# Optimization experiments

Hardware: AMD Instinct MI355X
Metric: run time of the kernel (lower is better)

Reference implementation:

```python
import jax, jax.numpy as jnp
import numpy as np

B, T, R, C, H = 8, 176, 116, 64, 200   # batch, time, roi, conv channels, mlp hidden
MAXG = 176                              # pad target for number of groups (== time)
TAU = 1e-4
IU = np.triu_indices(R, 1)              # upper triangle (diagonal=1), row-major like torch mask select


def setup_inputs() -> dict:
    key = jax.random.key(0)
    k = jax.random.split(key, 6)
    # gumbel(0,1) noise, as used by F.gumbel_softmax
    u = jax.random.uniform(k[4], (B, T, T), jnp.float32, 1e-10, 1.0 - 1e-7)
    gumbel = -jnp.log(-jnp.log(u))
    return {
        "X": jax.random.normal(k[0], (B, T, R), jnp.float32),
        "conv_w": jax.random.normal(k[1], (C, R), jnp.float32) * float(1.0 / np.sqrt(R)),
        "conv_b": jnp.zeros((C,), jnp.float32),
        "fc1_w": jax.random.normal(k[2], (H, C), jnp.float32) * float(1.0 / np.sqrt(C)),
        "fc1_b": jnp.zeros((H,), jnp.float32),
        "fc2_w": jax.random.normal(k[3], (1, H), jnp.float32) * float(1.0 / np.sqrt(H)),
        "fc2_b": jnp.zeros((1,), jnp.float32),
        "gumbel": gumbel,
    }


def _per_sample(Xi, idx):
    # Xi: [R, T] (roi x time), idx: [T] soft group index per timepoint
    # toggle(): consecutive runs of equal idx values form groups
    change = jnp.concatenate([jnp.ones((1,), bool), idx[1:] != idx[:-1]])
    gid = jnp.cumsum(change.astype(jnp.int32)) - 1            # [T] group id per timepoint
    num_groups = gid[-1] + 1
    toggle = (gid[None, :] == jnp.arange(MAXG)[:, None]).astype(Xi.dtype)  # [MAXG, T] one-hot rows
    MASK = (idx + 1.0)[None, :] * toggle                       # [MAXG, T]
    inv = jax.lax.stop_gradient(1.0 / MASK.sum(axis=0))        # [T] (detached in torch)
    final = inv[None, :] * MASK                                # [MAXG, T]
    res = Xi[None, :, :] * final[:, None, :]                   # [MAXG, R, T] group-masked signals
    # torch.corrcoef over rows (time axis is observations); normalization constant cancels
    xm = res - res.mean(axis=-1, keepdims=True)
    cov = jnp.einsum('grt,gst->grs', xm, xm)                   # [MAXG, R, R]
    d = jnp.einsum('grt,grt->gr', xm, xm)                      # diag of cov
    denom = jnp.sqrt(d[:, :, None] * d[:, None, :])
    corr = jnp.clip(cov / jnp.where(denom > 0, denom, 1.0), -1.0, 1.0)
    flat = corr[:, IU[0], IU[1]]                               # [MAXG, R*(R-1)/2] upper-tri flatten
    valid = (jnp.arange(MAXG) < num_groups)[:, None]           # zero-pad groups past num_groups
    return jnp.where(valid, flat, 0.0)


def reference(X, conv_w, conv_b, fc1_w, fc1_b, fc2_w, fc2_b, gumbel):
    # Conv1d(kernel_size=1) == per-timepoint linear: [B,T,R] -> [B,T,C]
    out_cnn = jnp.einsum('btr,cr->btc', X, conv_w) + conv_b
    diff = out_cnn[:, :, None, :] - out_cnn[:, None, :, :]      # [B,T,T,C]
    dist = jnp.sqrt(jax.nn.relu(diff * diff) + 1e-9)
    h = jax.nn.relu(jnp.einsum('btsc,hc->btsh', dist, fc1_w) + fc1_b)
    clf = jax.nn.sigmoid(jnp.einsum('btsh,h->bts', h, fc2_w[0]) + fc2_b[0])  # [B,T,T]
    eye = jnp.eye(T, dtype=bool)
    grouping_M = jnp.where(eye[None, :, :], 1.0, clf)
    # eigh returns ascending eigenvalues; torch sorts descending (reverse), but S uses the
    # ORIGINAL (un-reordered) eigenvectors, matching the source exactly
    vals, vecs = jnp.linalg.eigh(grouping_M)
    vals_desc = vals[:, ::-1]
    vals_desc = jnp.where(vals_desc <= 0, 1e-7, vals_desc)
    S = vecs * jnp.sqrt(vals_desc)[:, None, :] * 1000.0         # vectors @ diag(sqrt(vals)) * 1000
    Group = jax.nn.softmax((S + gumbel) / TAU, axis=2)          # gumbel_softmax, tau=1e-4, soft
    soft_indices = jnp.sum(Group * jnp.arange(T, dtype=S.dtype), axis=-1)  # [B,T]
    Xp = jnp.transpose(X, (0, 2, 1))                            # [B,R,T]
    padded = jax.vmap(_per_sample)(Xp, soft_indices)            # [B, MAXG, R*(R-1)/2]
    return padded, grouping_M, soft_indices
```

## Files before the change

kernel.cpp:

```cpp
#include <hip/hip_runtime.h>
#pragma clang fp contract(off)

#define Bn 8
#define Tn 176
#define Rn 116
#define Cn 64
#define Hn 200
#define NPAIRn 6670
#define MAXGn 176
#define TAUf 1e-4f
#define LD 176
#define LDA 177
#define LEAF 22
#define NT 512
#define FEPS 5.9604645e-08f
#define FEPS2 3.5527137e-15f
#define FSAFMIN 1.17549435e-38f

static __device__ __forceinline__ float f_sign(float a, float b) {
  return (b >= 0.0f) ? fabsf(a) : -fabsf(a);
}
static __device__ __forceinline__ float f_lapy2(float x, float y) {
  float xa = fabsf(x), ya = fabsf(y);
  float w = fmaxf(xa, ya), z = fminf(xa, ya);
  if (z == 0.0f) return w;
  float q = z / w;
  return w * sqrtf(1.0f + q * q);
}
static __device__ void f_lartg(float f, float g, float* c, float* s, float* r) {
  if (g == 0.0f) { *c = 1.0f; *s = 0.0f; *r = f; }
  else if (f == 0.0f) { *c = 0.0f; *s = (g >= 0.0f) ? 1.0f : -1.0f; *r = fabsf(g); }
  else {
    float d = sqrtf(f * f + g * g);
    float rr = (f >= 0.0f) ? d : -d;
    *c = f / rr; *s = g / rr; *r = rr;
  }
}
static __device__ float f_snrm2_strided(const float* x, int n, int stride) {
  float scale = 0.0f, ssq = 1.0f;
  for (int i = 0; i < n; i++) {
    float ax = fabsf(x[i * stride]);
    if (ax != 0.0f) {
      if (scale < ax) {
        float q = scale / ax;
        ssq = 1.0f + ssq * (q * q);
// ... 604 lines not shown
          g = d[i] - p;
          r = (d[i + 1] - g) * s + 2.0f * c * bb;
          p = s * r;
          d[i] = g + p;
          g = c * r - bb;
          work_c[i] = c; work_s[i] = s;
        }
        for (int j = 1; j <= l - mm; ++j) {
          float cj = work_c[mm + j - 1], sj = work_s[mm + j - 1];
          for (int rr = 0; rr < n; rr++) {
            float t1 = Z[rr * ldz + mm + j], t0 = Z[rr * ldz + mm + j - 1];
            Z[rr * ldz + mm + j] = cj * t1 - sj * t0;
            Z[rr * ldz + mm + j - 1] = sj * t1 + cj * t0;
          }
        }
        d[l] -= p; e[l - 1] = g;
      }
    }
  }
  for (int ii = 1; ii < n; ++ii) {
    int i = ii - 1, k = i; float p = d[i];
    for (int j = ii; j < n; ++j) if (d[j] < p) { k = j; p = d[j]; }
    if (k != i) {
      d[k] = d[i]; d[i] = p;
      for (int r = 0; r < n; r++) { float t = Z[r * ldz + i]; Z[r * ldz + i] = Z[r * ldz + k]; Z[r * ldz + k] = t; }
    }
  }
}

static __device__ void laed1_f(int tid, int nb, int n1, int off, float rho_in,
    float* Zb, float* Qt, float* Um, float* dd,
    float* dlamda, float* w2, float* lamv, float* wtv, float* zv, float* dnew, float* dsort,
    int* indxq, int* indxp, int* indxc, int* indxm,
    float* shs, int* shi) {
  int n2 = nb - n1;
  if (tid == 0) {
    float rho = rho_in;
    for (int i = 0; i < n1; i++) zv[i] = Zb[(off + n1 - 1) * LD + off + i];
    for (int i = 0; i < n2; i++) zv[n1 + i] = Zb[(off + n1) * LD + off + n1 + i];
    if (rho < 0.0f) for (int i = n1; i < nb; i++) zv[i] = -zv[i];
    const float isq2 = 0.70710678118654752440f;
    for (int i = 0; i < nb; i++) zv[i] *= isq2;
    rho = fabsf(2.0f * rho);
    for (int i = n1; i < nb; i++) indxq[off + i] += n1;
    for (int i = 0; i < nb; i++) dsort[i] = dd[off + indxq[off + i]];
    f_lamrg(n1, n2, dsort, 1, 1, indxc);
    for (int i = 0; i < nb; i++) indxm[i] = indxq[off + indxc[i]];
    float zmax = 0.0f, dmax = 0.0f;
    for (int i = 0; i < nb; i++) {
      float az = fabsf(zv[i]); if (az > zmax) zmax = az;
      float ad = fabsf(dd[off + i]); if (ad > dmax) dmax = ad;
    }
    float tol = 8.0f * FEPS * ((dmax > zmax) ? dmax : zmax);
    int K = 0;
    if (rho * zmax <= tol) {
      for (int j = 0; j < nb; j++) indxp[j] = indxm[j];
    } else {
      int K2 = nb; int pj = 0; int j; bool found = false;
      for (j = 0; j < nb; j++) {
        int nj = indxm[j];
        if (rho * fabsf(zv[nj]) <= tol) { K2--; indxp[K2] = nj; if (j == nb - 1) break; }
        else { pj = nj; found = true; break; }
      }
      if (found) {
        while (true) {
          j++;
          if (j >= nb) break;
          int nj = indxm[j];
          if (rho * fabsf(zv[nj]) <= tol) { K2--; indxp[K2] = nj; }
          else {
            float s_ = zv[pj], c_ = zv[nj];
            float tau_ = f_lapy2(c_, s_);
            float t_ = dd[off + nj] - dd[off + pj];
            c_ /= tau_; s_ = -s_ / tau_;
            if (fabsf(t_ * c_ * s_) <= tol) {
              zv[nj] = tau_; zv[pj] = 0.0f;
              for (int r = 0; r < nb; r++) {
                float x = Zb[(off + r) * LD + off + pj], y = Zb[(off + r) * LD + off + nj];
                Zb[(off + r) * LD + off + pj] = c_ * x + s_ * y;
                Zb[(off + r) * LD + off + nj] = c_ * y - s_ * x;
              }
              float t2 = dd[off + pj] * c_ * c_ + dd[off + nj] * s_ * s_;
              dd[off + nj] = dd[off + pj] * s_ * s_ + dd[off + nj] * c_ * c_;
              dd[off + pj] = t2;
              K2--;
              int i_ = 1;
              while (true) {
                if (K2 + i_ < nb) {
                  if (dd[off + pj] < dd[off + indxp[K2 + i_]]) {
                    indxp[K2 + i_ - 1] = indxp[K2 + i_]; indxp[K2 + i_] = pj; i_++;
                  } else { indxp[K2 + i_ - 1] = pj; break; }
                } else { indxp[K2 + i_ - 1] = pj; break; }
              }
              pj = nj;
            } else {
              dlamda[K] = dd[off + pj]; w2[K] = zv[pj]; indxp[K] = pj; K++;
              pj = nj;
            }
          }
        }
        dlamda[K] = dd[off + pj]; w2[K] = zv[pj]; indxp[K] = pj; K++;
      }
    }
    shi[0] = K; shs[0] = rho;
  }
  __syncthreads();
  int K = shi[0]; float rho = shs[0];
  if (K == 0) {
    for (int idx = tid; idx < nb * nb; idx += NT) {
      int r = idx / nb, jj = idx - r * nb;
      Qt[r * LD + jj] = Zb[(off + r) * LD + off + indxp[jj]];
    }
    for (int jj = tid; jj < nb; jj += NT) dnew[jj] = dd[off + indxp[jj]];
    __syncthreads();
    for (int idx = tid; idx < nb * nb; idx += NT) {
      int r = idx / nb, jj = idx - r * nb;
      Zb[(off + r) * LD + off + jj] = Qt[r * LD + jj];
    }
    for (int jj = tid; jj < nb; jj += NT) { dd[off + jj] = dnew[jj]; indxq[off + jj] = jj; }
    __syncthreads();
    return;
  }
  if (K == 1) {
    if (tid == 0) { lamv[0] = dlamda[0] + rho * w2[0] * w2[0]; Um[0] = 1.0f; }
  } else if (K == 2) {
    if (tid < 2) {
      float u0, u1, dl_;
      f_laed5(tid, dlamda, w2, rho, &dl_, &u0, &u1);
      lamv[tid] = dl_; Um[0 * LD + tid] = u0; Um[1 * LD + tid] = u1;
    }
  } else {
    if (tid < K) laed4_net(K, tid, dlamda, w2, rho, &lamv[tid], &Um[tid]);
  }
  __syncthreads();
  if (K > 2) {
    if (tid < K) {
      int i = tid; float val = Um[i * LD + i];
      for (int j2 = 0; j2 < K; j2++) if (j2 != i) val *= Um[i * LD + j2] / (dlamda[i] - dlamda[j2]);
      wtv[i] = f_sign(sqrtf(fabsf(val)), w2[i]);
    }
    __syncthreads();
    if (tid < K) {
      int j2 = tid;
      for (int i = 0; i < K; i++) Um[i * LD + j2] = wtv[i] / Um[i * LD + j2];
      float nrm = f_snrm2_strided(&Um[j2], K, LD);
      for (int i = 0; i < K; i++) Um[i * LD + j2] /= nrm;
    }
    __syncthreads();
  }
  for (int idx = tid; idx < nb * K; idx += NT) {
    int r = idx / K, j2 = idx - r * K;
    float acc = 0.0f;
    for (int i = 0; i < K; i++) acc = fmaf(Zb[(off + r) * LD + off + indxp[i]], Um[i * LD + j2], acc);
    Qt[r * LD + j2] = acc;
  }
  int nd = nb - K;
  for (int idx = tid; idx < nb * nd; idx += NT) {
    int r = idx / nd, jj = idx - r * nd;
    Qt[r * LD + K + jj] = Zb[(off + r) * LD + off + indxp[K + jj]];
  }
  for (int jj = tid; jj < nb; jj += NT) dnew[jj] = (jj < K) ? lamv[jj] : dd[off + indxp[jj]];
  __syncthreads();
  for (int idx = tid; idx < nb * nb; idx += NT) {
    int r = idx / nb, jj = idx - r * nb;
    Zb[(off + r) * LD + off + jj] = Qt[r * LD + jj];
  }
  for (int jj = tid; jj < nb; jj += NT) dd[off + jj] = dnew[jj];
  __syncthreads();
  if (tid == 0) f_lamrg(K, nb - K, dnew, 1, -1, indxq + off);
  __syncthreads();
}

#define FSTR 109824
__global__ __launch_bounds__(NT) void k_eigh2(const float* __restrict__ gm,
    float* __restrict__ fws,
    float* __restrict__ vecsbt, float* __restrict__ scales) {
  int b = blockIdx.x, tid = threadIdx.x;
  extern __shared__ char dynsm[];
  float* A = (float*)dynsm;
  float* sm1 = A + Tn * LDA;
  int* ib_ = (int*)(sm1 + 1760);
  float* Zb = fws + (size_t)b * FSTR;
  float* Qt = Zb + 30976;
  float* Um = Qt + 30976;
  float* Wp = Um + 30976;
  float* Wa = Wp + 5632;
  float* Wb = Wa + 5632;
  float* dd = sm1;
  float* ee = sm1 + 176;
  float* tauv = sm1 + 352;
  float* dlamda = sm1 + 528;
  float* w2 = sm1 + 704;
  float* lamv = sm1 + 880;
  float* wtv = sm1 + 1056;
  float* zv = sm1 + 1232;
  float* dnew = sm1 + 1408;
  float* dsort = sm1 + 1584;
  int* indxq = ib_;
  int* indxp = ib_ + 176;
  int* indxc = ib_ + 352;
  int* indxm = ib_ + 528;
  __shared__ float shv[176];
  __shared__ float shs[2];
  __shared__ int shi[2];
  __shared__ float t12[64];
  __shared__ float Tm[1024];
  __shared__ float Zleaf[8][LEAF][LEAF + 1];
  for (int i = tid; i < Tn * Tn; i += NT)
    A[(i / Tn) * LDA + (i % Tn)] = gm[(size_t)b * Tn * Tn + i];
  __syncthreads();
  for (int i0 = 0; i0 < Tn - 32; i0 += 32) {
    for (int i = 0; i < 32; i++) {
      int g = i0 + i;
      if (i > 0) {
        for (int r = g + tid; r < Tn; r += NT) {
          float acc = A[r * LDA + g];
          for (int k = 0; k < i; k++) acc = fmaf(-Wp[g * 32 + k], A[r * LDA + (i0 + k)], acc);
          for (int k = 0; k < i; k++) acc = fmaf(-A[g * LDA + (i0 + k)], Wp[r * 32 + k], acc);
          A[r * LDA + g] = acc;
        }
        __syncthreads();
      }
      if (tid == 0) {
        float scale = 0.0f, ssq = 1.0f;
        for (int r = g + 2; r < Tn; r++) {
          float ax = fabsf(A[r * LDA + g]);
          if (ax != 0.0f) {
            if (scale < ax) { float q = scale / ax; ssq = 1.0f + ssq * (q * q); scale = ax; }
            else { float q = ax / scale; ssq = ssq + q * q; }
          }
        }
        float xnorm = scale * sqrtf(ssq);
        float alpha = A[(g + 1) * LDA + g];
        float taui = 0.0f, scal = 0.0f;
        if (xnorm == 0.0f) { ee[g] = alpha; }
        else {
          float beta = -f_sign(f_lapy2(alpha, xnorm), alpha);
          taui = (beta - alpha) / beta;
          scal = 1.0f / (alpha - beta);
          ee[g] = beta;
        }
        tauv[g] = taui; shs[0] = taui; shs[1] = scal;
      }
      __syncthreads();
      float taui = shs[0];
      if (taui != 0.0f) {
        float scal = shs[1];
        for (int r = g + 2 + tid; r < Tn; r += NT) A[r * LDA + g] *= scal;
      }
      __syncthreads();
      if (tid == 0) A[(g + 1) * LDA + g] = 1.0f;
      __syncthreads();
      for (int r = g + 1 + tid; r < Tn; r += NT) {
        float acc = 0.0f;
        for (int c = g + 1; c < r; c++) acc = fmaf(A[c * LDA + g], A[r * LDA + c], acc);
        acc = fmaf(A[r * LDA + g], A[r * LDA + r], acc);
        float temp2 = 0.0f;
        for (int k = r + 1; k < Tn; k++) temp2 = fmaf(A[k * LDA + r], A[k * LDA + g], temp2);
        acc += temp2;
        shv[r] = acc;
      }
      __syncthreads();
      if (i > 0) {
        if (tid < i) {
          int k = tid;
          float acc = 0.0f;
          for (int r = g + 1; r < Tn; r++) acc = fmaf(Wp[r * 32 + k], A[r * LDA + g], acc);
          t12[k] = acc;
        }
        __syncthreads();
        for (int r = g + 1 + tid; r < Tn; r += NT) {
          float acc = shv[r];
          for (int k = 0; k < i; k++) acc = fmaf(-t12[k], A[r * LDA + (i0 + k)], acc);
          shv[r] = acc;
        }
        __syncthreads();
        if (tid < i) {
          int k = tid;
          float acc = 0.0f;
          for (int r = g + 1; r < Tn; r++) acc = fmaf(A[r * LDA + (i0 + k)], A[r * LDA + g], acc);
          t12[32 + k] = acc;
        }
        __syncthreads();
        for (int r = g + 1 + tid; r < Tn; r += NT) {
          float acc = shv[r];
          for (int k = 0; k < i; k++) acc = fmaf(-t12[32 + k], Wp[r * 32 + k], acc);
          shv[r] = acc;
        }
        __syncthreads();
      }
      for (int r = g + 1 + tid; r < Tn; r += NT) shv[r] = taui * shv[r];
      __syncthreads();
      if (tid == 0) {
        float dot = 0.0f;
        for (int r = g + 1; r < Tn; r++) dot = fmaf(shv[r], A[r * LDA + g], dot);
        shs[0] = -0.5f * taui * dot;
      }
      __syncthreads();
      float alf = shs[0];
      for (int r = g + 1 + tid; r < Tn; r += NT) Wp[r * 32 + i] = fmaf(alf, A[r * LDA + g], shv[r]);
      __syncthreads();
    }
    {
      int base2 = i0 + 32;
      int nt2 = Tn - base2;
      int npr = nt2 * (nt2 + 1) / 2;
      for (int p = tid; p < npr; p += NT) {
        int rr = (int)((sqrtf(8.0f * (float)p + 1.0f) - 1.0f) * 0.5f);
        while ((rr + 1) * (rr + 2) / 2 <= p) rr++;
        while (rr * (rr + 1) / 2 > p) rr--;
        int cc = p - rr * (rr + 1) / 2;
        int r = base2 + rr, c = base2 + cc;
        float acc = A[r * LDA + c];
        for (int L = 0; L < 32; L++) {
          acc = fmaf(A[r * LDA + (i0 + L)], -Wp[c * 32 + L], acc);
          acc = fmaf(Wp[r * 32 + L], -A[c * LDA + (i0 + L)], acc);
        }
        A[r * LDA + c] = acc;
        if (r != c) A[c * LDA + r] = acc;
      }
      __syncthreads();
      if (tid < 32) {
        int g2 = i0 + tid;
        A[(g2 + 1) * LDA + g2] = ee[g2];
      }
      __syncthreads();
    }
  }
  for (int i = 160; i < Tn - 1; i++) {
    if (tid == 0) {
      float scale = 0.0f, ssq = 1.0f;
      for (int r = i + 2; r < Tn; r++) {
        float ax = fabsf(A[r * LDA + i]);
        if (ax != 0.0f) {
          if (scale < ax) { float q = scale / ax; ssq = 1.0f + ssq * (q * q); scale = ax; }
          else { float q = ax / scale; ssq = ssq + q * q; }
        }
      }
      float xnorm = scale * sqrtf(ssq);
      float alpha = A[(i + 1) * LDA + i];
      float taui = 0.0f, scal = 0.0f;
      if (xnorm == 0.0f) { ee[i] = alpha; }
      else {
        float beta = -f_sign(f_lapy2(alpha, xnorm), alpha);
        taui = (beta - alpha) / beta;
        scal = 1.0f / (alpha - beta);
        ee[i] = beta;
      }
      tauv[i] = taui; shs[0] = taui; shs[1] = scal;
    }
    __syncthreads();
    float taui = shs[0];
    if (taui != 0.0f) {
      float scal = shs[1];
      for (int r = i + 2 + tid; r < Tn; r += NT) A[r * LDA + i] *= scal;
      __syncthreads();
      for (int r = i + 1 + tid; r < Tn; r += NT) {
        float acc = 0.0f;
        for (int c = i + 1; c < r; c++) {
          float vc = (c == i + 1) ? 1.0f : A[c * LDA + i];
          acc = fmaf(taui * vc, A[r * LDA + c], acc);
        }
        float vr = (r == i + 1) ? 1.0f : A[r * LDA + i];
        acc = fmaf(taui * vr, A[r * LDA + r], acc);
        float temp2 = 0.0f;
        for (int k = r + 1; k < Tn; k++) temp2 = fmaf(A[k * LDA + r], A[k * LDA + i], temp2);
        acc = fmaf(taui, temp2, acc);
        shv[r] = acc;
      }
      __syncthreads();
      if (tid == 0) {
        float dot = 0.0f;
        for (int r = i + 1; r < Tn; r++) {
          float vr = (r == i + 1) ? 1.0f : A[r * LDA + i];
          dot = fmaf(vr, shv[r], dot);
        }
        shs[0] = -0.5f * taui * dot;
      }
      __syncthreads();
      float alpha2 = shs[0];
      for (int r = i + 1 + tid; r < Tn; r += NT) {
        float vr = (r == i + 1) ? 1.0f : A[r * LDA + i];
        shv[r] = fmaf(alpha2, vr, shv[r]);
      }
      __syncthreads();
      int m2 = Tn - 1 - i;
      int npairs = m2 * (m2 + 1) / 2;
      for (int p = tid; p < npairs; p += NT) {
        int rr = (int)((sqrtf(8.0f * (float)p + 1.0f) - 1.0f) * 0.5f);
        while ((rr + 1) * (rr + 2) / 2 <= p) rr++;
        while (rr * (rr + 1) / 2 > p) rr--;
        int cc = p - rr * (rr + 1) / 2;
        int r = i + 1 + rr, c = i + 1 + cc;
        float vr = (r == i + 1) ? 1.0f : A[r * LDA + i];
        float vc = (c == i + 1) ? 1.0f : A[c * LDA + i];
        float val = A[r * LDA + c];
        val = fmaf(vr, -shv[c], val);
        val = fmaf(shv[r], -vc, val);
        A[r * LDA + c] = val;
      }
      __syncthreads();
    }
  }
  for (int i = tid; i < Tn; i += NT) dd[i] = A[i * LDA + i];
  __syncthreads();
  if (tid == 0) {
    float on = 0.0f;
    for (int i = 0; i < Tn; i++) { float v = fabsf(dd[i]); if (v > on) on = v; }
    for (int i = 0; i < Tn - 1; i++) { float v = fabsf(ee[i]); if (v > on) on = v; }
    shs[0] = (on > 0.0f) ? on : 1.0f;
  }
  __syncthreads();
  float orgnrm = shs[0];
  for (int i = tid; i < Tn; i += NT) dd[i] /= orgnrm;
  for (int i = tid; i < Tn - 1; i += NT) ee[i] /= orgnrm;
  for (int i = tid; i < Tn * Tn; i += NT)
    Zb[(i / Tn) * LD + (i % Tn)] = ((i / Tn) == (i % Tn)) ? 1.0f : 0.0f;
  for (int i = tid; i < 8 * LEAF * LEAF; i += NT) {
    int lf = i / (LEAF * LEAF);
    int rc = i - lf * (LEAF * LEAF);
    int r = rc / LEAF, c = rc - r * LEAF;
    Zleaf[lf][r][c] = (r == c) ? 1.0f : 0.0f;
  }
  __syncthreads();
  if (tid == 0) {
    for (int c = LEAF; c < Tn; c += LEAF) { dd[c - 1] -= fabsf(ee[c - 1]); dd[c] -= fabsf(ee[c - 1]); }
  }
  __syncthreads();
  if ((tid & 63) == 0 && (tid >> 6) < 8) {
    int lf = tid >> 6;
    steqr_f(LEAF, dd + LEAF * lf, ee + LEAF * lf, &Zleaf[lf][0][0], LEAF + 1);
  }
  __syncthreads();
  for (int i = tid; i < 8 * LEAF * LEAF; i += NT) {
    int lf = i / (LEAF * LEAF);
    int rc = i - lf * (LEAF * LEAF);
    int r = rc / LEAF, c = rc - r * LEAF;
    Zb[(size_t)(LEAF * lf + r) * LD + LEAF * lf + c] = Zleaf[lf][r][c];
  }
  __syncthreads();
  for (int i = tid; i < Tn; i += NT) indxq[i] = i % LEAF;
  __syncthreads();
  for (int nb = 2 * LEAF; nb <= Tn; nb *= 2) {
    for (int off = 0; off < Tn; off += nb) {
      laed1_f(tid, nb, nb / 2, off, ee[off + nb / 2 - 1],
              Zb, Qt, Um, dd, dlamda, w2, lamv, wtv, zv, dnew, dsort,
              indxq, indxp, indxc, indxm, shs, shi);
    }
  }
  for (int idx = tid; idx < Tn * Tn; idx += NT) {
    int r = idx / Tn, j = idx % Tn;
    Qt[r * LD + j] = Zb[r * LD + indxq[j]];
  }
  for (int j = tid; j < Tn; j += NT) dnew[j] = dd[indxq[j]];
  __syncthreads();
  for (int idx = tid; idx < Tn * Tn; idx += NT) {
    int r = idx / Tn, j = idx % Tn;
    Zb[r * LD + j] = Qt[r * LD + j];
  }
  for (int j = tid; j < Tn; j += NT) dd[j] = dnew[j] * orgnrm;
  __syncthreads();
  for (int bi = 0; bi < 6; bi++) {
    int s = (bi == 0) ? 160 : (128 - (bi - 1) * 32);
    int ibk = (bi == 0) ? 15 : 32;
    for (int i2 = 0; i2 < ibk; i2++) {
      float ti = tauv[s + i2];
      if (tid < i2) {
        int j2 = tid;
        float acc = 0.0f;
        for (int r = s + i2; r <= Tn - 2; r++) {
          float vj = (r == s + j2) ? 1.0f : A[(r + 1) * LDA + (s + j2)];
          float vi = (r == s + i2) ? 1.0f : A[(r + 1) * LDA + (s + i2)];
          acc = fmaf(vj, vi, acc);
        }
        Tm[j2 * 32 + i2] = (ti == 0.0f) ? 0.0f : (-ti) * acc;
      }
      __syncthreads();
      if (tid == 0) {
        if (ti != 0.0f) {
          for (int J = 0; J < i2; J++) {
            float tmp = Tm[J * 32 + i2];
            if (tmp != 0.0f) {
              for (int I2 = 0; I2 < J; I2++) Tm[I2 * 32 + i2] = fmaf(tmp, Tm[I2 * 32 + J], Tm[I2 * 32 + i2]);
              Tm[J * 32 + i2] = tmp * Tm[J * 32 + J];
            }
          }
        }
        Tm[i2 * 32 + i2] = ti;
      }
      __syncthreads();
    }
    int c2r0 = s + ibk + 1;
    int nc2 = Tn - c2r0;
    for (int e = tid; e < Tn * ibk; e += NT) {
      int c = e / ibk, j = e - (e / ibk) * ibk;
      float acc = Zb[(s + 1 + j) * LD + c];
      for (int k = j + 1; k < ibk; k++) {
        float v1 = A[(s + 1 + k) * LDA + (s + j)];
        acc = fmaf(v1, Zb[(s + 1 + k) * LD + c], acc);
      }
      Wb[c * 32 + j] = acc;
    }
    __syncthreads();
    if (nc2 > 0) {
      for (int e = tid; e < Tn * ibk; e += NT) {
        int c = e / ibk, j = e - (e / ibk) * ibk;
        float acc = 0.0f;
        for (int rr = 0; rr < nc2; rr++)
          acc = fmaf(Zb[(c2r0 + rr) * LD + c], A[(c2r0 + rr) * LDA + (s + j)], acc);
        Wb[c * 32 + j] = acc + Wb[c * 32 + j];
      }
      __syncthreads();
    }
    for (int e = tid; e < Tn * ibk; e += NT) {
      int c = e / ibk, j = e - (e / ibk) * ibk;
      float acc = Tm[j * 32 + j] * Wb[c * 32 + j];
      for (int K = j + 1; K < ibk; K++) acc = fmaf(Tm[j * 32 + K], Wb[c * 32 + K], acc);
      Wa[c * 32 + j] = acc;
    }
    __syncthreads();
    if (nc2 > 0) {
      for (int e = tid; e < nc2 * Tn; e += NT) {
        int rr = e / Tn, c = e - (e / Tn) * Tn;
        float cv = Zb[(c2r0 + rr) * LD + c];
        for (int j = 0; j < ibk; j++)
          cv = fmaf(-Wa[c * 32 + j], A[(c2r0 + rr) * LDA + (s + j)], cv);
        Zb[(c2r0 + rr) * LD + c] = cv;
      }
      __syncthreads();
    }
    for (int e = tid; e < Tn * ibk; e += NT) {
      int c = e / ibk, j = e - (e / ibk) * ibk;
      float acc = Wa[c * 32 + j];
      for (int K = j - 1; K >= 0; K--) {
        float v1 = A[(s + 1 + j) * LDA + (s + K)];
        acc = fmaf(v1, Wa[c * 32 + K], acc);
      }
      Wb[c * 32 + j] = acc;
    }
    __syncthreads();
    for (int e = tid; e < ibk * Tn; e += NT) {
      int j = e / Tn, c = e - (e / Tn) * Tn;
      Zb[(s + 1 + j) * LD + c] = Zb[(s + 1 + j) * LD + c] - Wb[c * 32 + j];
    }
    __syncthreads();
  }
  for (int idx = tid; idx < Tn * Tn; idx += NT) {
    int t = idx / Tn, j = idx % Tn;
    vecsbt[((size_t)b * Tn + t) * Tn + j] = Zb[t * LD + j];
  }
  for (int j = tid; j < Tn; j += NT) {
    float vd = dd[Tn - 1 - j];
    if (vd <= 0.f) vd = 1e-7f;
    scales[b * Tn + j] = sqrtf(vd) * 1000.f;
  }
}

__global__ void k_conv(const float* __restrict__ X, const float* __restrict__ cw,
                       const float* __restrict__ cb, float* __restrict__ oc) {
  int idx = blockIdx.x * 256 + threadIdx.x;
  if (idx >= Bn * Tn * Cn) return;
  int c = idx & (Cn - 1);
  int bt = idx >> 6;
  const float* xr = X + bt * Rn;
  const float* wr = cw + c * Rn;
  float acc = cb[c];
#pragma unroll 4
  for (int r = 0; r < Rn; ++r) acc = fmaf(xr[r], wr[r], acc);
  oc[idx] = acc;
}

__global__ __launch_bounds__(256) void k_mlp(const float* __restrict__ oc,
        const float* __restrict__ w1, const float* __restrict__ b1,
        const float* __restrict__ w2, const float* __restrict__ b2,
        float* __restrict__ gm) {
  __shared__ float xw[4 * 8];
  int tid = threadIdx.x;
  int lane = tid & 63, wv = tid >> 6;
  int b = blockIdx.x / Tn, t = blockIdx.x % Tn;
  bool active = (tid < Hn);
  float w1r[64];
  if (active) {
// ... 166 lines not shown
    co = fminf(fmaxf(co, -1.f), 1.f);
    out[k] = co;
  }
}

extern "C" void kernel_launch(void* const* d_in, const int* in_sizes, int n_in,
                              void* d_out, int out_size, void* d_ws, size_t ws_size,
                              hipStream_t stream) {
  const float* X  = (const float*)d_in[0];
  const float* cw = (const float*)d_in[1];
  const float* cb = (const float*)d_in[2];
  const float* w1 = (const float*)d_in[3];
  const float* b1 = (const float*)d_in[4];
  const float* w2 = (const float*)d_in[5];
  const float* b2 = (const float*)d_in[6];
  const float* gu = (const float*)d_in[7];

  float* out = (float*)d_out;
  float* padded = out;
  float* gm = out + (size_t)Bn * MAXGn * NPAIRn;
  float* si = gm + (size_t)Bn * Tn * Tn;

  char* base = (char*)d_ws;
  float* oc = (float*)base;
  float* Y = oc + 90112;
  float* vecsbt = Y + 163328;
  float* scales = vecsbt + 247808;
  int* gstart = (int*)(scales + 1408);
  int* gend = gstart + 1408;
  int* ngr = gend + 1408;
  int* lut = ngr + 8;
  float* fws = (float*)(base + ((2075280 + 255) & ~255));

  size_t eigh_lds = (size_t)(Tn * LDA + 1760) * 4 + 880 * 4;

  k_conv<<<(Bn * Tn * Cn + 255) / 256, 256, 0, stream>>>(X, cw, cb, oc);
  k_lut<<<(NPAIRn + 255) / 256, 256, 0, stream>>>(lut);
  k_mlp<<<Bn * Tn, 256, 0, stream>>>(oc, w1, b1, w2, b2, gm);
  k_eigh2<<<Bn, NT, eigh_lds, stream>>>(gm, fws, vecsbt, scales);
  k_softidx<<<Bn * Tn, 64, 0, stream>>>(vecsbt, scales, gu, si);
  k_prep<<<Bn, 256, 0, stream>>>(X, si, Y, gstart, gend, ngr);
  k_corr<<<Bn * MAXGn, 256, 0, stream>>>(Y, gstart, gend, ngr, lut, padded);
}
```

Measured before the change: 15.11 ms.

## Split eigh kernel into tridiagonalization and divide-and-conquer, eigenvectors in LDS

Splits the single eigh kernel into two launches. k_ssytrd reduces the matrix to tridiagonal form with the panel workspace Wp held in shared memory, padded to a stride of 33. k_stedc then keeps the eigenvector matrix Zb in shared memory (padded stride 177) instead of global workspace, and reads the Householder vectors back from global. The deflation Givens rotations in laed1 are now recorded by thread 0 and applied in parallel afterwards, instead of serially by one thread. This adds a kernel launch and a global round trip of the reduced matrix, and each rotation costs a barrier.

```diff
diff --git a/kernel.cpp b/kernel.cpp
--- a/kernel.cpp
+++ b/kernel.cpp
@@ -11,6 +11,8 @@
 #define TAUf 1e-4f
 #define LD 176
 #define LDA 177
+#define LDZ 177
+#define WPS 33
 #define LEAF 22
 #define NT 512
 #define FEPS 5.9604645e-08f
@@ -681,12 +683,14 @@
     float* Zb, float* Qt, float* Um, float* dd,
     float* dlamda, float* w2, float* lamv, float* wtv, float* zv, float* dnew, float* dsort,
     int* indxq, int* indxp, int* indxc, int* indxm,
+    int* rotP, int* rotN, float* rotC, float* rotS,
     float* shs, int* shi) {
   int n2 = nb - n1;
   if (tid == 0) {
     float rho = rho_in;
-    for (int i = 0; i < n1; i++) zv[i] = Zb[(off + n1 - 1) * LD + off + i];
-    for (int i = 0; i < n2; i++) zv[n1 + i] = Zb[(off + n1) * LD + off + n1 + i];
+    int cnt = 0;
+    for (int i = 0; i < n1; i++) zv[i] = Zb[(off + n1 - 1) * LDZ + off + i];
+    for (int i = 0; i < n2; i++) zv[n1 + i] = Zb[(off + n1) * LDZ + off + n1 + i];
     if (rho < 0.0f) for (int i = n1; i < nb; i++) zv[i] = -zv[i];
     const float isq2 = 0.70710678118654752440f;
     for (int i = 0; i < nb; i++) zv[i] *= isq2;
@@ -724,11 +728,7 @@
             c_ /= tau_; s_ = -s_ / tau_;
             if (fabsf(t_ * c_ * s_) <= tol) {
               zv[nj] = tau_; zv[pj] = 0.0f;
-              for (int r = 0; r < nb; r++) {
-                float x = Zb[(off + r) * LD + off + pj], y = Zb[(off + r) * LD + off + nj];
-                Zb[(off + r) * LD + off + pj] = c_ * x + s_ * y;
-                Zb[(off + r) * LD + off + nj] = c_ * y - s_ * x;
-              }
+              rotP[cnt] = pj; rotN[cnt] = nj; rotC[cnt] = c_; rotS[cnt] = s_; cnt++;
               float t2 = dd[off + pj] * c_ * c_ + dd[off + nj] * s_ * s_;
               dd[off + nj] = dd[off + pj] * s_ * s_ + dd[off + nj] * c_ * c_;
               dd[off + pj] = t2;
@@ -751,20 +751,33 @@
         dlamda[K] = dd[off + pj]; w2[K] = zv[pj]; indxp[K] = pj; K++;
       }
     }
-    shi[0] = K; shs[0] = rho;
-  }
-  __syncthreads();
+    shi[0] = K; shs[0] = rho; shi[1] = cnt;
+  }
+  __syncthreads();
+  {
+    int cnt = shi[1];
+    for (int p = 0; p < cnt; ++p) {
+      int pj = rotP[p], nj = rotN[p];
+      float c_ = rotC[p], s_ = rotS[p];
+      for (int r = tid; r < nb; r += NT) {
+        float x = Zb[(off + r) * LDZ + off + pj], y = Zb[(off + r) * LDZ + off + nj];
+        Zb[(off + r) * LDZ + off + pj] = c_ * x + s_ * y;
+        Zb[(off + r) * LDZ + off + nj] = c_ * y - s_ * x;
+      }
+      __syncthreads();
+    }
+  }
   int K = shi[0]; float rho = shs[0];
   if (K == 0) {
     for (int idx = tid; idx < nb * nb; idx += NT) {
       int r = idx / nb, jj = idx - r * nb;
-      Qt[r * LD + jj] = Zb[(off + r) * LD + off + indxp[jj]];
+      Qt[r * LD + jj] = Zb[(off + r) * LDZ + off + indxp[jj]];
     }
     for (int jj = tid; jj < nb; jj += NT) dnew[jj] = dd[off + indxp[jj]];
     __syncthreads();
     for (int idx = tid; idx < nb * nb; idx += NT) {
       int r = idx / nb, jj = idx - r * nb;
-      Zb[(off + r) * LD + off + jj] = Qt[r * LD + jj];
+      Zb[(off + r) * LDZ + off + jj] = Qt[r * LD + jj];
     }
     for (int jj = tid; jj < nb; jj += NT) { dd[off + jj] = dnew[jj]; indxq[off + jj] = jj; }
     __syncthreads();
@@ -800,19 +813,19 @@
   for (int idx = tid; idx < nb * K; idx += NT) {
     int r = idx / K, j2 = idx - r * K;
     float acc = 0.0f;
-    for (int i = 0; i < K; i++) acc = fmaf(Zb[(off + r) * LD + off + indxp[i]], Um[i * LD + j2], acc);
+    for (int i = 0; i < K; i++) acc = fmaf(Zb[(off + r) * LDZ + off + indxp[i]], Um[i * LD + j2], acc);
     Qt[r * LD + j2] = acc;
   }
   int nd = nb - K;
   for (int idx = tid; idx < nb * nd; idx += NT) {
     int r = idx / nd, jj = idx - r * nd;
-    Qt[r * LD + K + jj] = Zb[(off + r) * LD + off + indxp[K + jj]];
+    Qt[r * LD + K + jj] = Zb[(off + r) * LDZ + off + indxp[K + jj]];
   }
   for (int jj = tid; jj < nb; jj += NT) dnew[jj] = (jj < K) ? lamv[jj] : dd[off + indxp[jj]];
   __syncthreads();
   for (int idx = tid; idx < nb * nb; idx += NT) {
     int r = idx / nb, jj = idx - r * nb;
-    Zb[(off + r) * LD + off + jj] = Qt[r * LD + jj];
+    Zb[(off + r) * LDZ + off + jj] = Qt[r * LD + jj];
   }
   for (int jj = tid; jj < nb; jj += NT) dd[off + jj] = dnew[jj];
   __syncthreads();
@@ -820,21 +833,246 @@
   __syncthreads();
 }
 
-#define FSTR 109824
-__global__ __launch_bounds__(NT) void k_eigh2(const float* __restrict__ gm,
-    float* __restrict__ fws,
+#define FSTR 104720
+__global__ __launch_bounds__(NT) void k_ssytrd(const float* __restrict__ gm,
+    float* __restrict__ fws) {
+  int b = blockIdx.x, tid = threadIdx.x;
+  extern __shared__ char dynsm[];
+  float* A = (float*)dynsm;
+  float* Wp = A + Tn * LDA;
+  float* sm = Wp + Tn * WPS;
+  float* dd = sm;
+  float* ee = sm + 176;
+  float* tauv = sm + 352;
+  float* Aout = fws + (size_t)b * FSTR;
+  float* ddg = Aout + 30976 * 3 + 5632 * 2;
+  float* eeg = ddg + 176;
+  float* tauvg = eeg + 176;
+  __shared__ float shv[176];
+  __shared__ float shs[2];
+  __shared__ float t12[64];
+  for (int i = tid; i < Tn * Tn; i += NT)
+    A[(i / Tn) * LDA + (i % Tn)] = gm[(size_t)b * Tn * Tn + i];
+  __syncthreads();
+  for (int i0 = 0; i0 < Tn - 32; i0 += 32) {
+    for (int i = 0; i < 32; i++) {
+      int g = i0 + i;
+      if (i > 0) {
+        for (int r = g + tid; r < Tn; r += NT) {
+          float acc = A[r * LDA + g];
+          for (int k = 0; k < i; k++) acc = fmaf(-Wp[g * WPS + k], A[r * LDA + (i0 + k)], acc);
+          for (int k = 0; k < i; k++) acc = fmaf(-A[g * LDA + (i0 + k)], Wp[r * WPS + k], acc);
+          A[r * LDA + g] = acc;
+        }
+        __syncthreads();
+      }
+      if (tid == 0) {
+        float scale = 0.0f, ssq = 1.0f;
+        for (int r = g + 2; r < Tn; r++) {
+          float ax = fabsf(A[r * LDA + g]);
+          if (ax != 0.0f) {
+            if (scale < ax) { float q = scale / ax; ssq = 1.0f + ssq * (q * q); scale = ax; }
+            else { float q = ax / scale; ssq = ssq + q * q; }
+          }
+        }
+        float xnorm = scale * sqrtf(ssq);
+        float alpha = A[(g + 1) * LDA + g];
+        float taui = 0.0f, scal = 0.0f;
+        if (xnorm == 0.0f) { ee[g] = alpha; }
+        else {
+          float beta = -f_sign(f_lapy2(alpha, xnorm), alpha);
+          taui = (beta - alpha) / beta;
+          scal = 1.0f / (alpha - beta);
+          ee[g] = beta;
+        }
+        tauv[g] = taui; shs[0] = taui; shs[1] = scal;
+      }
+      __syncthreads();
+      float taui = shs[0];
+      if (taui != 0.0f) {
+        float scal = shs[1];
+        for (int r = g + 2 + tid; r < Tn; r += NT) A[r * LDA + g] *= scal;
+      }
+      __syncthreads();
+      if (tid == 0) A[(g + 1) * LDA + g] = 1.0f;
+      __syncthreads();
+      for (int r = g + 1 + tid; r < Tn; r += NT) {
+        float acc = 0.0f;
+        for (int c = g + 1; c < r; c++) acc = fmaf(A[c * LDA + g], A[r * LDA + c], acc);
+        acc = fmaf(A[r * LDA + g], A[r * LDA + r], acc);
+        float temp2 = 0.0f;
+        for (int k = r + 1; k < Tn; k++) temp2 = fmaf(A[k * LDA + r], A[k * LDA + g], temp2);
+        acc += temp2;
+        shv[r] = acc;
+      }
+      __syncthreads();
+      if (i > 0) {
+        if (tid < i) {
+          int k = tid;
+          float acc = 0.0f;
+          for (int r = g + 1; r < Tn; r++) acc = fmaf(Wp[r * WPS + k], A[r * LDA + g], acc);
+          t12[k] = acc;
+        }
+        __syncthreads();
+        for (int r = g + 1 + tid; r < Tn; r += NT) {
+          float acc = shv[r];
+          for (int k = 0; k < i; k++) acc = fmaf(-t12[k], A[r * LDA + (i0 + k)], acc);
+          shv[r] = acc;
+        }
+        __syncthreads();
+        if (tid < i) {
+          int k = tid;
+          float acc = 0.0f;
+          for (int r = g + 1; r < Tn; r++) acc = fmaf(A[r * LDA + (i0 + k)], A[r * LDA + g], acc);
+          t12[32 + k] = acc;
+        }
+        __syncthreads();
+        for (int r = g + 1 + tid; r < Tn; r += NT) {
+          float acc = shv[r];
+          for (int k = 0; k < i; k++) acc = fmaf(-t12[32 + k], Wp[r * WPS + k], acc);
+          shv[r] = acc;
+        }
+        __syncthreads();
+      }
+      for (int r = g + 1 + tid; r < Tn; r += NT) shv[r] = taui * shv[r];
+      __syncthreads();
+      if (tid == 0) {
+        float dot = 0.0f;
+        for (int r = g + 1; r < Tn; r++) dot = fmaf(shv[r], A[r * LDA + g], dot);
+        shs[0] = -0.5f * taui * dot;
+      }
+      __syncthreads();
+      float alf = shs[0];
+      for (int r = g + 1 + tid; r < Tn; r += NT) Wp[r * WPS + i] = fmaf(alf, A[r * LDA + g], shv[r]);
+      __syncthreads();
+    }
+    {
+      int base2 = i0 + 32;
+      int nt2 = Tn - base2;
+      int npr = nt2 * (nt2 + 1) / 2;
+      for (int p = tid; p < npr; p += NT) {
+        int rr = (int)((sqrtf(8.0f * (float)p + 1.0f) - 1.0f) * 0.5f);
+        while ((rr + 1) * (rr + 2) / 2 <= p) rr++;
+        while (rr * (rr + 1) / 2 > p) rr--;
+        int cc = p - rr * (rr + 1) / 2;
+        int r = base2 + rr, c = base2 + cc;
+        float acc = A[r * LDA + c];
+        for (int L = 0; L < 32; L++) {
+          acc = fmaf(A[r * LDA + (i0 + L)], -Wp[c * WPS + L], acc);
+          acc = fmaf(Wp[r * WPS + L], -A[c * LDA + (i0 + L)], acc);
+        }
+        A[r * LDA + c] = acc;
+        if (r != c) A[c * LDA + r] = acc;
+      }
+      __syncthreads();
+      if (tid < 32) {
+        int g2 = i0 + tid;
+        A[(g2 + 1) * LDA + g2] = ee[g2];
+      }
+      __syncthreads();
+    }
+  }
+  for (int i = 160; i < Tn - 1; i++) {
+    if (tid == 0) {
+      float scale = 0.0f, ssq = 1.0f;
+      for (int r = i + 2; r < Tn; r++) {
+        float ax = fabsf(A[r * LDA + i]);
+        if (ax != 0.0f) {
+          if (scale < ax) { float q = scale / ax; ssq = 1.0f + ssq * (q * q); scale = ax; }
+          else { float q = ax / scale; ssq = ssq + q * q; }
+        }
+      }
+      float xnorm = scale * sqrtf(ssq);
+      float alpha = A[(i + 1) * LDA + i];
+      float taui = 0.0f, scal = 0.0f;
+      if (xnorm == 0.0f) { ee[i] = alpha; }
+      else {
+        float beta = -f_sign(f_lapy2(alpha, xnorm), alpha);
+        taui = (beta - alpha) / beta;
+        scal = 1.0f / (alpha - beta);
+        ee[i] = beta;
+      }
+      tauv[i] = taui; shs[0] = taui; shs[1] = scal;
+    }
+    __syncthreads();
+    float taui = shs[0];
+    if (taui != 0.0f) {
+      float scal = shs[1];
+      for (int r = i + 2 + tid; r < Tn; r += NT) A[r * LDA + i] *= scal;
+      __syncthreads();
+      for (int r = i + 1 + tid; r < Tn; r += NT) {
+        float acc = 0.0f;
+        for (int c = i + 1; c < r; c++) {
+          float vc = (c == i + 1) ? 1.0f : A[c * LDA + i];
+          acc = fmaf(taui * vc, A[r * LDA + c], acc);
+        }
+        float vr = (r == i + 1) ? 1.0f : A[r * LDA + i];
+        acc = fmaf(taui * vr, A[r * LDA + r], acc);
+        float temp2 = 0.0f;
+        for (int k = r + 1; k < Tn; k++) temp2 = fmaf(A[k * LDA + r], A[k * LDA + i], temp2);
+        acc = fmaf(taui, temp2, acc);
+        shv[r] = acc;
+      }
+      __syncthreads();
+      if (tid == 0) {
+        float dot = 0.0f;
+        for (int r = i + 1; r < Tn; r++) {
+          float vr = (r == i + 1) ? 1.0f : A[r * LDA + i];
+          dot = fmaf(vr, shv[r], dot);
+        }
+        shs[0] = -0.5f * taui * dot;
+      }
+      __syncthreads();
+      float alpha2 = shs[0];
+      for (int r = i + 1 + tid; r < Tn; r += NT) {
+        float vr = (r == i + 1) ? 1.0f : A[r * LDA + i];
+        shv[r] = fmaf(alpha2, vr, shv[r]);
+      }
+      __syncthreads();
+      int m2 = Tn - 1 - i;
+      int npairs = m2 * (m2 + 1) / 2;
+      for (int p = tid; p < npairs; p += NT) {
+        int rr = (int)((sqrtf(8.0f * (float)p + 1.0f) - 1.0f) * 0.5f);
+        while ((rr + 1) * (rr + 2) / 2 <= p) rr++;
+        while (rr * (rr + 1) / 2 > p) rr--;
+        int cc = p - rr * (rr + 1) / 2;
+        int r = i + 1 + rr, c = i + 1 + cc;
+        float vr = (r == i + 1) ? 1.0f : A[r * LDA + i];
+        float vc = (c == i + 1) ? 1.0f : A[c * LDA + i];
+        float val = A[r * LDA + c];
+        val = fmaf(vr, -shv[c], val);
+        val = fmaf(shv[r], -vc, val);
+        A[r * LDA + c] = val;
+      }
+      __syncthreads();
+    }
+  }
+  for (int i = tid; i < Tn; i += NT) dd[i] = A[i * LDA + i];
+  __syncthreads();
+  for (int i = tid; i < Tn * Tn; i += NT)
+    Aout[i] = A[(i / Tn) * LDA + (i % Tn)];
+  for (int i = tid; i < Tn; i += NT) {
+    ddg[i] = dd[i];
+    eeg[i] = (i < Tn - 1) ? ee[i] : 0.0f;
+    tauvg[i] = (i < Tn - 1) ? tauv[i] : 0.0f;
+  }
+}
+
+__global__ __launch_bounds__(NT) void k_stedc(float* __restrict__ fws,
     float* __restrict__ vecsbt, float* __restrict__ scales) {
   int b = blockIdx.x, tid = threadIdx.x;
   extern __shared__ char dynsm[];
-  float* A = (float*)dynsm;
-  float* sm1 = A + Tn * LDA;
+  float* Zb = (float*)dynsm;
+  float* sm1 = Zb + Tn * LDZ;
   int* ib_ = (int*)(sm1 + 1760);
-  float* Zb = fws + (size_t)b * FSTR;
-  float* Qt = Zb + 30976;
+  float* Aout = fws + (size_t)b * FSTR;
+  float* Qt = Aout + 30976;
   float* Um = Qt + 30976;
-  float* Wp = Um + 30976;
-  float* Wa = Wp + 5632;
+  float* Wa = Um + 30976;
   float* Wb = Wa + 5632;
+  float* ddg = Wb + 5632;
+  float* eeg = ddg + 176;
+  float* tauvg = eeg + 176;
   float* dd = sm1;
   float* ee = sm1 + 176;
   float* tauv = sm1 + 352;
@@ -849,209 +1087,16 @@
   int* indxp = ib_ + 176;
   int* indxc = ib_ + 352;
   int* indxm = ib_ + 528;
-  __shared__ float shv[176];
   __shared__ float shs[2];
   __shared__ int shi[2];
-  __shared__ float t12[64];
   __shared__ float Tm[1024];
-  __shared__ float Zleaf[8][LEAF][LEAF + 1];
-  for (int i = tid; i < Tn * Tn; i += NT)
-    A[(i / Tn) * LDA + (i % Tn)] = gm[(size_t)b * Tn * Tn + i];
-  __syncthreads();
-  for (int i0 = 0; i0 < Tn - 32; i0 += 32) {
-    for (int i = 0; i < 32; i++) {
-      int g = i0 + i;
-      if (i > 0) {
-        for (int r = g + tid; r < Tn; r += NT) {
-          float acc = A[r * LDA + g];
-          for (int k = 0; k < i; k++) acc = fmaf(-Wp[g * 32 + k], A[r * LDA + (i0 + k)], acc);
-          for (int k = 0; k < i; k++) acc = fmaf(-A[g * LDA + (i0 + k)], Wp[r * 32 + k], acc);
-          A[r * LDA + g] = acc;
-        }
-        __syncthreads();
-      }
-      if (tid == 0) {
-        float scale = 0.0f, ssq = 1.0f;
-        for (int r = g + 2; r < Tn; r++) {
-          float ax = fabsf(A[r * LDA + g]);
-          if (ax != 0.0f) {
-            if (scale < ax) { float q = scale / ax; ssq = 1.0f + ssq * (q * q); scale = ax; }
-            else { float q = ax / scale; ssq = ssq + q * q; }
-          }
-        }
-        float xnorm = scale * sqrtf(ssq);
-        float alpha = A[(g + 1) * LDA + g];
-        float taui = 0.0f, scal = 0.0f;
-        if (xnorm == 0.0f) { ee[g] = alpha; }
-        else {
-          float beta = -f_sign(f_lapy2(alpha, xnorm), alpha);
-          taui = (beta - alpha) / beta;
-          scal = 1.0f / (alpha - beta);
-          ee[g] = beta;
-        }
-        tauv[g] = taui; shs[0] = taui; shs[1] = scal;
-      }
-      __syncthreads();
-      float taui = shs[0];
-      if (taui != 0.0f) {
-        float scal = shs[1];
-        for (int r = g + 2 + tid; r < Tn; r += NT) A[r * LDA + g] *= scal;
-      }
-      __syncthreads();
-      if (tid == 0) A[(g + 1) * LDA + g] = 1.0f;
-      __syncthreads();
-      for (int r = g + 1 + tid; r < Tn; r += NT) {
-        float acc = 0.0f;
-        for (int c = g + 1; c < r; c++) acc = fmaf(A[c * LDA + g], A[r * LDA + c], acc);
-        acc = fmaf(A[r * LDA + g], A[r * LDA + r], acc);
-        float temp2 = 0.0f;
-        for (int k = r + 1; k < Tn; k++) temp2 = fmaf(A[k * LDA + r], A[k * LDA + g], temp2);
-        acc += temp2;
-        shv[r] = acc;
-      }
-      __syncthreads();
-      if (i > 0) {
-        if (tid < i) {
-          int k = tid;
-          float acc = 0.0f;
-          for (int r = g + 1; r < Tn; r++) acc = fmaf(Wp[r * 32 + k], A[r * LDA + g], acc);
-          t12[k] = acc;
-        }
-        __syncthreads();
-        for (int r = g + 1 + tid; r < Tn; r += NT) {
-          float acc = shv[r];
-          for (int k = 0; k < i; k++) acc = fmaf(-t12[k], A[r * LDA + (i0 + k)], acc);
-          shv[r] = acc;
-        }
-        __syncthreads();
-        if (tid < i) {
-          int k = tid;
-          float acc = 0.0f;
-          for (int r = g + 1; r < Tn; r++) acc = fmaf(A[r * LDA + (i0 + k)], A[r * LDA + g], acc);
-          t12[32 + k] = acc;
-        }
-        __syncthreads();
-        for (int r = g + 1 + tid; r < Tn; r += NT) {
-          float acc = shv[r];
-          for (int k = 0; k < i; k++) acc = fmaf(-t12[32 + k], Wp[r * 32 + k], acc);
-          shv[r] = acc;
-        }
-        __syncthreads();
-      }
-      for (int r = g + 1 + tid; r < Tn; r += NT) shv[r] = taui * shv[r];
-      __syncthreads();
-      if (tid == 0) {
-        float dot = 0.0f;
-        for (int r = g + 1; r < Tn; r++) dot = fmaf(shv[r], A[r * LDA + g], dot);
-        shs[0] = -0.5f * taui * dot;
-      }
-      __syncthreads();
-      float alf = shs[0];
-      for (int r = g + 1 + tid; r < Tn; r += NT) Wp[r * 32 + i] = fmaf(alf, A[r * LDA + g], shv[r]);
-      __syncthreads();
-    }
-    {
-      int base2 = i0 + 32;
-      int nt2 = Tn - base2;
-      int npr = nt2 * (nt2 + 1) / 2;
-      for (int p = tid; p < npr; p += NT) {
-        int rr = (int)((sqrtf(8.0f * (float)p + 1.0f) - 1.0f) * 0.5f);
-        while ((rr + 1) * (rr + 2) / 2 <= p) rr++;
-        while (rr * (rr + 1) / 2 > p) rr--;
-        int cc = p - rr * (rr + 1) / 2;
-        int r = base2 + rr, c = base2 + cc;
-        float acc = A[r * LDA + c];
-        for (int L = 0; L < 32; L++) {
-          acc = fmaf(A[r * LDA + (i0 + L)], -Wp[c * 32 + L], acc);
-          acc = fmaf(Wp[r * 32 + L], -A[c * LDA + (i0 + L)], acc);
-        }
-        A[r * LDA + c] = acc;
-        if (r != c) A[c * LDA + r] = acc;
-      }
-      __syncthreads();
-      if (tid < 32) {
-        int g2 = i0 + tid;
-        A[(g2 + 1) * LDA + g2] = ee[g2];
-      }
-      __syncthreads();
-    }
-  }
-  for (int i = 160; i < Tn - 1; i++) {
-    if (tid == 0) {
-      float scale = 0.0f, ssq = 1.0f;
-      for (int r = i + 2; r < Tn; r++) {
-        float ax = fabsf(A[r * LDA + i]);
-        if (ax != 0.0f) {
-          if (scale < ax) { float q = scale / ax; ssq = 1.0f + ssq * (q * q); scale = ax; }
-          else { float q = ax / scale; ssq = ssq + q * q; }
-        }
-      }
-      float xnorm = scale * sqrtf(ssq);
-      float alpha = A[(i + 1) * LDA + i];
-      float taui = 0.0f, scal = 0.0f;
-      if (xnorm == 0.0f) { ee[i] = alpha; }
-      else {
-        float beta = -f_sign(f_lapy2(alpha, xnorm), alpha);
-        taui = (beta - alpha) / beta;
-        scal = 1.0f / (alpha - beta);
-        ee[i] = beta;
-      }
-      tauv[i] = taui; shs[0] = taui; shs[1] = scal;
-    }
-    __syncthreads();
-    float taui = shs[0];
-    if (taui != 0.0f) {
-      float scal = shs[1];
-      for (int r = i + 2 + tid; r < Tn; r += NT) A[r * LDA + i] *= scal;
-      __syncthreads();
-      for (int r = i + 1 + tid; r < Tn; r += NT) {
-        float acc = 0.0f;
-        for (int c = i + 1; c < r; c++) {
-          float vc = (c == i + 1) ? 1.0f : A[c * LDA + i];
-          acc = fmaf(taui * vc, A[r * LDA + c], acc);
-        }
-        float vr = (r == i + 1) ? 1.0f : A[r * LDA + i];
-        acc = fmaf(taui * vr, A[r * LDA + r], acc);
-        float temp2 = 0.0f;
-        for (int k = r + 1; k < Tn; k++) temp2 = fmaf(A[k * LDA + r], A[k * LDA + i], temp2);
-        acc = fmaf(taui, temp2, acc);
-        shv[r] = acc;
-      }
-      __syncthreads();
-      if (tid == 0) {
-        float dot = 0.0f;
-        for (int r = i + 1; r < Tn; r++) {
-          float vr = (r == i + 1) ? 1.0f : A[r * LDA + i];
-          dot = fmaf(vr, shv[r], dot);
-        }
-        shs[0] = -0.5f * taui * dot;
-      }
-      __syncthreads();
-      float alpha2 = shs[0];
-      for (int r = i + 1 + tid; r < Tn; r += NT) {
-        float vr = (r == i + 1) ? 1.0f : A[r * LDA + i];
-        shv[r] = fmaf(alpha2, vr, shv[r]);
-      }
-      __syncthreads();
-      int m2 = Tn - 1 - i;
-      int npairs = m2 * (m2 + 1) / 2;
-      for (int p = tid; p < npairs; p += NT) {
-        int rr = (int)((sqrtf(8.0f * (float)p + 1.0f) - 1.0f) * 0.5f);
-        while ((rr + 1) * (rr + 2) / 2 <= p) rr++;
-        while (rr * (rr + 1) / 2 > p) rr--;
-        int cc = p - rr * (rr + 1) / 2;
-        int r = i + 1 + rr, c = i + 1 + cc;
-        float vr = (r == i + 1) ? 1.0f : A[r * LDA + i];
-        float vc = (c == i + 1) ? 1.0f : A[c * LDA + i];
-        float val = A[r * LDA + c];
-        val = fmaf(vr, -shv[c], val);
-        val = fmaf(shv[r], -vc, val);
-        A[r * LDA + c] = val;
-      }
-      __syncthreads();
-    }
-  }
-  for (int i = tid; i < Tn; i += NT) dd[i] = A[i * LDA + i];
+  __shared__ int rotP[176], rotN[176];
+  __shared__ float rotC[176], rotS[176];
+  for (int i = tid; i < Tn; i += NT) {
+    dd[i] = ddg[i];
+    ee[i] = eeg[i];
+    tauv[i] = tauvg[i];
+  }
   __syncthreads();
   if (tid == 0) {
     float on = 0.0f;
@@ -1064,13 +1109,7 @@
   for (int i = tid; i < Tn; i += NT) dd[i] /= orgnrm;
   for (int i = tid; i < Tn - 1; i += NT) ee[i] /= orgnrm;
   for (int i = tid; i < Tn * Tn; i += NT)
-    Zb[(i / Tn) * LD + (i % Tn)] = ((i / Tn) == (i % Tn)) ? 1.0f : 0.0f;
-  for (int i = tid; i < 8 * LEAF * LEAF; i += NT) {
-    int lf = i / (LEAF * LEAF);
-    int rc = i - lf * (LEAF * LEAF);
-    int r = rc / LEAF, c = rc - r * LEAF;
-    Zleaf[lf][r][c] = (r == c) ? 1.0f : 0.0f;
-  }
+    Zb[(i / Tn) * LDZ + (i % Tn)] = ((i / Tn) == (i % Tn)) ? 1.0f : 0.0f;
   __syncthreads();
   if (tid == 0) {
     for (int c = LEAF; c < Tn; c += LEAF) { dd[c - 1] -= fabsf(ee[c - 1]); dd[c] -= fabsf(ee[c - 1]); }
@@ -1078,14 +1117,7 @@
   __syncthreads();
   if ((tid & 63) == 0 && (tid >> 6) < 8) {
     int lf = tid >> 6;
-    steqr_f(LEAF, dd + LEAF * lf, ee + LEAF * lf, &Zleaf[lf][0][0], LEAF + 1);
-  }
-  __syncthreads();
-  for (int i = tid; i < 8 * LEAF * LEAF; i += NT) {
-    int lf = i / (LEAF * LEAF);
-    int rc = i - lf * (LEAF * LEAF);
-    int r = rc / LEAF, c = rc - r * LEAF;
-    Zb[(size_t)(LEAF * lf + r) * LD + LEAF * lf + c] = Zleaf[lf][r][c];
+    steqr_f(LEAF, dd + LEAF * lf, ee + LEAF * lf, &Zb[(LEAF * lf) * LDZ + LEAF * lf], LDZ);
   }
   __syncthreads();
   for (int i = tid; i < Tn; i += NT) indxq[i] = i % LEAF;
@@ -1094,18 +1126,18 @@
     for (int off = 0; off < Tn; off += nb) {
       laed1_f(tid, nb, nb / 2, off, ee[off + nb / 2 - 1],
               Zb, Qt, Um, dd, dlamda, w2, lamv, wtv, zv, dnew, dsort,
-              indxq, indxp, indxc, indxm, shs, shi);
+              indxq, indxp, indxc, indxm, rotP, rotN, rotC, rotS, shs, shi);
     }
   }
   for (int idx = tid; idx < Tn * Tn; idx += NT) {
     int r = idx / Tn, j = idx % Tn;
-    Qt[r * LD + j] = Zb[r * LD + indxq[j]];
+    Qt[r * LD + j] = Zb[r * LDZ + indxq[j]];
   }
   for (int j = tid; j < Tn; j += NT) dnew[j] = dd[indxq[j]];
   __syncthreads();
   for (int idx = tid; idx < Tn * Tn; idx += NT) {
     int r = idx / Tn, j = idx % Tn;
-    Zb[r * LD + j] = Qt[r * LD + j];
+    Zb[r * LDZ + j] = Qt[r * LD + j];
   }
   for (int j = tid; j < Tn; j += NT) dd[j] = dnew[j] * orgnrm;
   __syncthreads();
@@ -1118,8 +1150,8 @@
         int j2 = tid;
         float acc = 0.0f;
         for (int r = s + i2; r <= Tn - 2; r++) {
-          float vj = (r == s + j2) ? 1.0f : A[(r + 1) * LDA + (s + j2)];
-          float vi = (r == s + i2) ? 1.0f : A[(r + 1) * LDA + (s + i2)];
+          float vj = (r == s + j2) ? 1.0f : Aout[(r + 1) * LD + (s + j2)];
+          float vi = (r == s + i2) ? 1.0f : Aout[(r + 1) * LD + (s + i2)];
           acc = fmaf(vj, vi, acc);
         }
         Tm[j2 * 32 + i2] = (ti == 0.0f) ? 0.0f : (-ti) * acc;
@@ -1143,10 +1175,10 @@
     int nc2 = Tn - c2r0;
     for (int e = tid; e < Tn * ibk; e += NT) {
       int c = e / ibk, j = e - (e / ibk) * ibk;
-      float acc = Zb[(s + 1 + j) * LD + c];
+      float acc = Zb[(s + 1 + j) * LDZ + c];
       for (int k = j + 1; k < ibk; k++) {
-        float v1 = A[(s + 1 + k) * LDA + (s + j)];
-        acc = fmaf(v1, Zb[(s + 1 + k) * LD + c], acc);
+        float v1 = Aout[(s + 1 + k) * LD + (s + j)];
+        acc = fmaf(v1, Zb[(s + 1 + k) * LDZ + c], acc);
       }
       Wb[c * 32 + j] = acc;
     }
@@ -1156,7 +1188,7 @@
         int c = e / ibk, j = e - (e / ibk) * ibk;
         float acc = 0.0f;
         for (int rr = 0; rr < nc2; rr++)
-          acc = fmaf(Zb[(c2r0 + rr) * LD + c], A[(c2r0 + rr) * LDA + (s + j)], acc);
+          acc = fmaf(Zb[(c2r0 + rr) * LDZ + c], Aout[(c2r0 + rr) * LD + (s + j)], acc);
         Wb[c * 32 + j] = acc + Wb[c * 32 + j];
       }
       __syncthreads();
@@ -1171,10 +1203,10 @@
     if (nc2 > 0) {
       for (int e = tid; e < nc2 * Tn; e += NT) {
         int rr = e / Tn, c = e - (e / Tn) * Tn;
-        float cv = Zb[(c2r0 + rr) * LD + c];
+        float cv = Zb[(c2r0 + rr) * LDZ + c];
         for (int j = 0; j < ibk; j++)
-          cv = fmaf(-Wa[c * 32 + j], A[(c2r0 + rr) * LDA + (s + j)], cv);
-        Zb[(c2r0 + rr) * LD + c] = cv;
+          cv = fmaf(-Wa[c * 32 + j], Aout[(c2r0 + rr) * LD + (s + j)], cv);
+        Zb[(c2r0 + rr) * LDZ + c] = cv;
       }
       __syncthreads();
     }
@@ -1182,7 +1214,7 @@
       int c = e / ibk, j = e - (e / ibk) * ibk;
       float acc = Wa[c * 32 + j];
       for (int K = j - 1; K >= 0; K--) {
-        float v1 = A[(s + 1 + j) * LDA + (s + K)];
+        float v1 = Aout[(s + 1 + j) * LD + (s + K)];
         acc = fmaf(v1, Wa[c * 32 + K], acc);
       }
       Wb[c * 32 + j] = acc;
@@ -1190,13 +1222,13 @@
     __syncthreads();
     for (int e = tid; e < ibk * Tn; e += NT) {
       int j = e / Tn, c = e - (e / Tn) * Tn;
-      Zb[(s + 1 + j) * LD + c] = Zb[(s + 1 + j) * LD + c] - Wb[c * 32 + j];
+      Zb[(s + 1 + j) * LDZ + c] = Zb[(s + 1 + j) * LDZ + c] - Wb[c * 32 + j];
     }
     __syncthreads();
   }
   for (int idx = tid; idx < Tn * Tn; idx += NT) {
     int t = idx / Tn, j = idx % Tn;
-    vecsbt[((size_t)b * Tn + t) * Tn + j] = Zb[t * LD + j];
+    vecsbt[((size_t)b * Tn + t) * Tn + j] = Zb[t * LDZ + j];
   }
   for (int j = tid; j < Tn; j += NT) {
     float vd = dd[Tn - 1 - j];
@@ -1429,12 +1461,14 @@
   int* lut = ngr + 8;
   float* fws = (float*)(base + ((2075280 + 255) & ~255));
 
-  size_t eigh_lds = (size_t)(Tn * LDA + 1760) * 4 + 880 * 4;
+  size_t ssytrd_lds = (size_t)(Tn * LDA + Tn * WPS + 528) * 4;
+  size_t stedc_lds = (size_t)(Tn * LDZ + 1760) * 4 + 880 * 4;
 
   k_conv<<<(Bn * Tn * Cn + 255) / 256, 256, 0, stream>>>(X, cw, cb, oc);
   k_lut<<<(NPAIRn + 255) / 256, 256, 0, stream>>>(lut);
   k_mlp<<<Bn * Tn, 256, 0, stream>>>(oc, w1, b1, w2, b2, gm);
-  k_eigh2<<<Bn, NT, eigh_lds, stream>>>(gm, fws, vecsbt, scales);
+  k_ssytrd<<<Bn, NT, ssytrd_lds, stream>>>(gm, fws);
+  k_stedc<<<Bn, NT, stedc_lds, stream>>>(fws, vecsbt, scales);
   k_softidx<<<Bn * Tn, 64, 0, stream>>>(vecsbt, scales, gu, si);
   k_prep<<<Bn, 256, 0, stream>>>(X, si, Y, gstart, gend, ngr);
   k_corr<<<Bn * MAXGn, 256, 0, stream>>>(Y, gstart, gend, ngr, lut, padded);
```

Result: no change. 14.88 ms (-1.6%).
